# Kernel optimization log

Hardware: AMD Instinct MI355X
Metric: run time of the kernel (lower is better)

Reference implementation:

```python
import jax, jax.numpy as jnp
import numpy as np

EMBED_DIM = 512
NUM_HEADS = 8
QKV_DIM = 64
MS_HIDDEN = 16
COST_DIMS = 1
SCORES_DIMS = COST_DIMS + 1  # dot-product score + cost-mat score


def setup_inputs() -> dict:
    key = jax.random.key(0)
    ks = jax.random.split(key, 12)
    B, R, C = 8, 256, 256
    row_emb = jax.random.normal(ks[0], (B, R, EMBED_DIM), dtype=jnp.float32)
    col_emb = jax.random.normal(ks[1], (B, C, EMBED_DIM), dtype=jnp.float32)
    cost_mat = jax.random.uniform(ks[2], (B, R, C, COST_DIMS), dtype=jnp.float32)
    attn_mask = jax.random.randint(ks[3], (B, R, C), 0, 2).astype(jnp.bool_)
    # learned params (stored [in, out]; torch Linear applies x @ W.T)
    s = 1.0 / np.sqrt(EMBED_DIM)
    Wq = jax.random.uniform(ks[4], (EMBED_DIM, NUM_HEADS * QKV_DIM), minval=-s, maxval=s)
    Wk = jax.random.uniform(ks[5], (EMBED_DIM, NUM_HEADS * QKV_DIM), minval=-s, maxval=s)
    Wv = jax.random.uniform(ks[6], (EMBED_DIM, NUM_HEADS * QKV_DIM), minval=-s, maxval=s)
    Wo = jax.random.uniform(ks[7], (EMBED_DIM, EMBED_DIM), minval=-s, maxval=s)
    m1 = np.sqrt(1.0 / SCORES_DIMS)
    m2 = np.sqrt(1.0 / MS_HIDDEN)
    W1 = jax.random.uniform(ks[8], (SCORES_DIMS * NUM_HEADS, MS_HIDDEN * NUM_HEADS), minval=-m1, maxval=m1)
    W2 = jax.random.uniform(ks[9], (MS_HIDDEN * NUM_HEADS, NUM_HEADS), minval=-m2, maxval=m2)
    alpha = jnp.ones((1, NUM_HEADS, 1, 1, 1), dtype=jnp.float32)
    return {"row_emb": row_emb, "col_emb": col_emb, "cost_mat": cost_mat,
            "attn_mask": attn_mask, "Wq": Wq, "Wk": Wk, "Wv": Wv, "Wo": Wo,
            "W1": W1, "W2": W2, "alpha": alpha}


def reference(row_emb, col_emb, cost_mat, attn_mask, Wq, Wk, Wv, Wo, W1, W2, alpha):
    B, R, E = row_emb.shape
    C = col_emb.shape[1]
    H, D = NUM_HEADS, QKV_DIM
    norm = 1.0 / jnp.sqrt(jnp.asarray(D, row_emb.dtype))
    # projections -> (b, h, s, d)
    q = (row_emb @ Wq).reshape(B, R, H, D).transpose(0, 2, 1, 3)
    k = (col_emb @ Wk).reshape(B, C, H, D).transpose(0, 2, 1, 3)
    v = (col_emb @ Wv).reshape(B, C, H, D).transpose(0, 2, 1, 3)
    dot = norm * jnp.einsum('bhrd,bhcd->bhrc', q, k)  # (B,H,R,C)
    # mixed-score MLP: concat dot score with alpha-scaled cost-mat score
    cm = alpha * cost_mat[:, None]                    # (B,H,R,C,COST_DIMS)
    scores = jnp.concatenate([dot[..., None], cm], axis=-1)  # (B,H,R,C,S)
    s = scores.transpose(0, 2, 3, 1, 4).reshape(B, R, C, H * SCORES_DIMS)
    mixed = jax.nn.relu(s @ W1) @ W2                  # (B,R,C,H)
    logits = mixed.transpose(0, 3, 1, 2)              # (B,H,R,C)
    # masked softmax (rows fully masked -> zero weights)
    mask = attn_mask[:, None]                         # (B,1,R,C)
    all_masked = jnp.all(mask, axis=-1, keepdims=True)
    logits = jnp.where(mask, -jnp.inf, logits)
    weights = jax.nn.softmax(logits, axis=-1)
    weights = jnp.where(all_masked, 0.0, weights)
    out = jnp.einsum('bhrc,bhcd->bhrd', weights, v)   # (B,H,R,D)
    out = out.transpose(0, 2, 1, 3).reshape(B, R, H * D)
    return out @ Wo
```

## Files before the change

### kernel.cpp

```cpp
#include <hip/hip_runtime.h>
#include <hip/hip_bf16.h>

#define B_ 8
#define R_ 256
#define C_ 256
#define H_ 8
#define D_ 64

typedef __attribute__((ext_vector_type(8))) short s8v;
typedef __attribute__((ext_vector_type(4))) short s4v;
typedef __attribute__((ext_vector_type(4))) float f4v;

static __device__ __forceinline__ unsigned short f2b(float x) {
    __hip_bfloat16 h = __float2bfloat16(x);
    return *reinterpret_cast<unsigned short*>(&h);
}
static __device__ __forceinline__ float b2f(unsigned short u) {
    union { unsigned int i; float f; } c;
    c.i = (unsigned int)u << 16;
    return c.f;
}

__global__ __launch_bounds__(256) void prep(
    const float* __restrict__ re, const float* __restrict__ ce,
    const float* __restrict__ W1, const float* __restrict__ W2,
    const float* __restrict__ alpha,
    unsigned short* __restrict__ reb, unsigned short* __restrict__ ceb,
    unsigned short* __restrict__ w1af, unsigned short* __restrict__ w2af)
{
    const int t = blockIdx.x * 256 + threadIdx.x;
    {
        float2 v = *(const float2*)&re[(size_t)t * 2];
        reb[t * 2]     = f2b(v.x);
        reb[t * 2 + 1] = f2b(v.y);
        float2 w = *(const float2*)&ce[(size_t)t * 2];
        ceb[t * 2]     = f2b(w.x);
        ceb[t * 2 + 1] = f2b(w.y);
    }
    if (blockIdx.x == 0) {
        const int l = threadIdx.x;
        for (int q = 0; q < 16; ++q) {
            const int idx = l * 16 + q;
            const int kk = idx & 7, lane = (idx >> 3) & 63, n = idx >> 9;
            const int j = n * 16 + (lane & 15);
            const int s = 8 * (lane >> 4) + kk;
            float val = 0.f;
            if (s < 16) {
                val = W1[(2 * (s >> 1)) * 128 + j];
            } else if (s < 18) {
                for (int h = 0; h < 8; ++h)
                    val += alpha[h] * W1[(2 * h + 1) * 128 + j];
            }
            w1af[idx] = f2b(val);
        }
        for (int q = 0; q < 8; ++q) {
            const int idx = l * 8 + q;
            const int kk = idx & 7, lane = (idx >> 3) & 63, kc = idx >> 9;
            const int h = lane & 15, g = lane >> 4;
            const int phi = 16 * (2 * kc + (kk >> 2)) + 4 * g + (kk & 3);
            w2af[idx] = f2b(h < 8 ? W2[phi * 8 + h] : 0.f);
        }
    }
}

__global__ __launch_bounds__(256) void prep_w(
    const float* __restrict__ Wq, const float* __restrict__ Wk,
    const float* __restrict__ Wv, const float* __restrict__ Wo,
    unsigned short* __restrict__ wqt, unsigned short* __restrict__ wkt,
    unsigned short* __restrict__ wvt, unsigned short* __restrict__ wot)
{
    __shared__ unsigned short ldsT[64][68];
    const int which = blockIdx.y;
    const float* W = which == 0 ? Wq : which == 1 ? Wk : which == 2 ? Wv : Wo;
    unsigned short* WT = which == 0 ? wqt : which == 1 ? wkt : which == 2 ? wvt : wot;
    const int k0 = (blockIdx.x & 7) * 64;
    const int n0 = (blockIdx.x >> 3) * 64;
    const int t = threadIdx.x;
    const int rn = t & 15;
    const int rk = t >> 4;
    #pragma unroll
    for (int i = 0; i < 4; ++i) {
        const int kk = rk + 16 * i;
        const float4 v = *(const float4*)&W[(size_t)(k0 + kk) * 512 + n0 + rn * 4];
        ldsT[rn * 4 + 0][kk] = f2b(v.x);
        ldsT[rn * 4 + 1][kk] = f2b(v.y);
        ldsT[rn * 4 + 2][kk] = f2b(v.z);
        ldsT[rn * 4 + 3][kk] = f2b(v.w);
    }
    __syncthreads();
    #pragma unroll
    for (int i = 0; i < 4; ++i) {
        const int nn = rk + 16 * i;
        const s4v r = *(const s4v*)&ldsT[nn][rn * 4];
        *(s4v*)&WT[(size_t)(n0 + nn) * 512 + k0 + rn * 4] = r;
    }
}

__global__ __launch_bounds__(256) void gemm_qkv(
    const unsigned short* __restrict__ reb, const unsigned short* __restrict__ ceb,
    const unsigned short* __restrict__ wqt, const unsigned short* __restrict__ wkt,
    const unsigned short* __restrict__ wvt,
    unsigned short* __restrict__ Qb, unsigned short* __restrict__ Kb,
    unsigned short* __restrict__ VT)
{
    const int z = blockIdx.z;
    const unsigned short* A;
    const unsigned short* Bm;
    int Ar0, Br0;
    if (z == 0)      { A = reb; Bm = wqt; Ar0 = blockIdx.x * 64; Br0 = blockIdx.y * 64; }
    else if (z == 1) { A = ceb; Bm = wkt; Ar0 = blockIdx.x * 64; Br0 = blockIdx.y * 64; }
    else             { A = wvt; Bm = ceb; Ar0 = blockIdx.y * 64; Br0 = blockIdx.x * 64; }

    const int t = threadIdx.x, lane = t & 63, wave = t >> 6;
    const int row0 = Ar0 + (wave >> 1) * 32;
    const int col0 = Br0 + (wave & 1) * 32;
    const int lr = lane & 15, ko = (lane >> 4) * 8;

    const unsigned short* Ap0 = A + (size_t)(row0 + lr) * 512 + ko;
    const unsigned short* Ap1 = Ap0 + 16 * 512;
    const unsigned short* Bp0 = Bm + (size_t)(col0 + lr) * 512 + ko;
    const unsigned short* Bp1 = Bp0 + 16 * 512;

    f4v acc[2][2] = {};
    #pragma unroll 4
    for (int k0 = 0; k0 < 512; k0 += 32) {
        s8v a0 = *(const s8v*)(Ap0 + k0);
        s8v a1 = *(const s8v*)(Ap1 + k0);
        s8v b0 = *(const s8v*)(Bp0 + k0);
        s8v b1 = *(const s8v*)(Bp1 + k0);
        acc[0][0] = __builtin_amdgcn_mfma_f32_16x16x32_bf16(a0, b0, acc[0][0], 0, 0, 0);
        acc[0][1] = __builtin_amdgcn_mfma_f32_16x16x32_bf16(a0, b1, acc[0][1], 0, 0, 0);
        acc[1][0] = __builtin_amdgcn_mfma_f32_16x16x32_bf16(a1, b0, acc[1][0], 0, 0, 0);
        acc[1][1] = __builtin_amdgcn_mfma_f32_16x16x32_bf16(a1, b1, acc[1][1], 0, 0, 0);
    }

    const float sc = (z == 0) ? 0.125f : 1.0f;
    const int rbase = (lane >> 4) * 4;
    #pragma unroll
    for (int i = 0; i < 2; ++i)
        #pragma unroll
        for (int j = 0; j < 2; ++j)
            #pragma unroll
            for (int reg = 0; reg < 4; ++reg) {
                const int rowIdx = row0 + i * 16 + rbase + reg;
                const int colIdx = col0 + j * 16 + lr;
                const unsigned short v = f2b(acc[i][j][reg] * sc);
                if (z == 0) {
                    Qb[(size_t)rowIdx * 512 + colIdx] = v;
                } else if (z == 1) {
                    const int b = rowIdx >> 8, c = rowIdx & 255;
                    const int h = colIdx >> 6, d = colIdx & 63;
                    Kb[(((size_t)b * 8 + h) * 256 + c) * 64 + d] = v;
                } else {
                    const int h = rowIdx >> 6, d = rowIdx & 63;
                    const int b = colIdx >> 8, c = colIdx & 255;
                    VT[(((size_t)b * 8 + h) * 64 + d) * 256 + c] = v;
                }
            }
}

__global__ __launch_bounds__(256) void gemm_out(
    const unsigned short* __restrict__ OHb, const unsigned short* __restrict__ wot,
    float* __restrict__ out)
{
    const int t = threadIdx.x, lane = t & 63, wave = t >> 6;
    const int row0 = blockIdx.x * 64 + (wave >> 1) * 32;
    const int col0 = blockIdx.y * 64 + (wave & 1) * 32;
    const int lr = lane & 15, ko = (lane >> 4) * 8;

    const unsigned short* Ap0 = OHb + (size_t)(row0 + lr) * 512 + ko;
    const unsigned short* Ap1 = Ap0 + 16 * 512;
    const unsigned short* Bp0 = wot + (size_t)(col0 + lr) * 512 + ko;
    const unsigned short* Bp1 = Bp0 + 16 * 512;

    f4v acc[2][2] = {};
    #pragma unroll 4
    for (int k0 = 0; k0 < 512; k0 += 32) {
        s8v a0 = *(const s8v*)(Ap0 + k0);
        s8v a1 = *(const s8v*)(Ap1 + k0);
        s8v b0 = *(const s8v*)(Bp0 + k0);
        s8v b1 = *(const s8v*)(Bp1 + k0);
        acc[0][0] = __builtin_amdgcn_mfma_f32_16x16x32_bf16(a0, b0, acc[0][0], 0, 0, 0);
        acc[0][1] = __builtin_amdgcn_mfma_f32_16x16x32_bf16(a0, b1, acc[0][1], 0, 0, 0);
        acc[1][0] = __builtin_amdgcn_mfma_f32_16x16x32_bf16(a1, b0, acc[1][0], 0, 0, 0);
        acc[1][1] = __builtin_amdgcn_mfma_f32_16x16x32_bf16(a1, b1, acc[1][1], 0, 0, 0);
    }

    const int rbase = (lane >> 4) * 4;
    #pragma unroll
    for (int i = 0; i < 2; ++i)
        #pragma unroll
        for (int j = 0; j < 2; ++j)
            #pragma unroll
            for (int reg = 0; reg < 4; ++reg)
                out[(size_t)(row0 + i * 16 + rbase + reg) * 512 + col0 + j * 16 + lr] =
                    acc[i][j][reg];
}

__global__ __launch_bounds__(512, 2) void attn_fused(
    const unsigned short* __restrict__ Qb,
    const unsigned short* __restrict__ Kb,
    const unsigned short* __restrict__ VT,
    const float* __restrict__ cost,
    const int* __restrict__ mask,
    const unsigned short* __restrict__ w1af,
    const unsigned short* __restrict__ w2af,
    unsigned short* __restrict__ OHb)
{
    __shared__ unsigned short dotb[4][256][24];
    __shared__ unsigned short w_t3[8][4][264];

    const int t    = threadIdx.x;
    const int lane = t & 63;
    const int w    = t >> 6;
    const int li   = lane & 15;
    const int g    = lane >> 4;
    const int b    = blockIdx.y;
    const int r0   = blockIdx.x * 4;

    {
        const int rr = lane & 3;
        const int ko = g * 8;
        const unsigned short* Qp = Qb + ((size_t)b * R_ + r0 + rr) * 512 + w * 64 + ko;
        const s8v a0 = *(const s8v*)Qp;
        const s8v a1 = *(const s8v*)(Qp + 32);
        const unsigned short* Kp = Kb + (((size_t)b * 8 + w) * 256) * 64;
        #pragma unroll
        for (int ct = 0; ct < 16; ++ct) {
            const unsigned short* Bp = Kp + (size_t)(ct * 16 + li) * 64 + ko;
            const s8v b0 = *(const s8v*)Bp;
            const s8v b1v = *(const s8v*)(Bp + 32);
            f4v acc = __builtin_amdgcn_mfma_f32_16x16x32_bf16(a0, b0, (f4v){0.f,0.f,0.f,0.f}, 0, 0, 0);
            acc = __builtin_amdgcn_mfma_f32_16x16x32_bf16(a1, b1v, acc, 0, 0, 0);
            if (lane < 16) {
                const int c = ct * 16 + lane;
                #pragma unroll
                for (int reg = 0; reg < 4; ++reg) {
                    const float x = acc[reg];
                    const unsigned short hi = f2b(x);
                    const unsigned short lo = f2b(x - b2f(hi));
                    *(unsigned int*)&dotb[reg][c][2 * w] =
                        (unsigned int)hi | ((unsigned int)lo << 16);
                }
            }
        }
    }
    __syncthreads();

    {
        s8v w1A[8], w2A[4];
        #pragma unroll
        for (int n = 0; n < 8; ++n) w1A[n] = ((const s8v*)w1af)[n * 64 + lane];
        #pragma unroll
        for (int kc = 0; kc < 4; ++kc) w2A[kc] = ((const s8v*)w2af)[kc * 64 + lane];

        const int r   = w & 3;
        const int ct0 = (w >> 2) * 8;
        const float* costRow = cost + ((size_t)b * R_ + r0 + r) * 256;

        #pragma unroll
        for (int i = 0; i < 8; ++i) {
            const int c = (ct0 + i) * 16 + li;
            s8v b1;
            {
                const s8v t0 = *(const s8v*)&dotb[r][c][(g & 1) * 8];
                const float cv = costRow[c];
                const unsigned short chi = f2b(cv);
                const unsigned short clo = f2b(cv - b2f(chi));
                if (g < 2) {
                    b1 = t0;
                } else if (g == 2) {
                    s8v bc = {0, 0, 0, 0, 0, 0, 0, 0};
                    bc[0] = (short)chi; bc[1] = (short)clo;
                    b1 = bc;
                } else {
                    s8v bz = {0, 0, 0, 0, 0, 0, 0, 0};
                    b1 = bz;
                }
            }
            unsigned int pk[16];
            #pragma unroll
            for (int n = 0; n < 8; ++n) {
                f4v acc = __builtin_amdgcn_mfma_f32_16x16x32_bf16(
                    w1A[n], b1, (f4v){0.f,0.f,0.f,0.f}, 0, 0, 0);
                const float a0 = fmaxf(acc[0], 0.f), a1 = fmaxf(acc[1], 0.f);
                const float a2 = fmaxf(acc[2], 0.f), a3 = fmaxf(acc[3], 0.f);
                pk[2 * n]     = (unsigned int)f2b(a0) | ((unsigned int)f2b(a1) << 16);
                pk[2 * n + 1] = (unsigned int)f2b(a2) | ((unsigned int)f2b(a3) << 16);
            }
            f4v acc2 = (f4v){0.f, 0.f, 0.f, 0.f};
            #pragma unroll
            for (int kc = 0; kc < 4; ++kc) {
                union { s8v v; unsigned int u[4]; } bb;
                bb.u[0] = pk[4 * kc + 0];
                bb.u[1] = pk[4 * kc + 1];
                bb.u[2] = pk[4 * kc + 2];
                bb.u[3] = pk[4 * kc + 3];
                acc2 = __builtin_amdgcn_mfma_f32_16x16x32_bf16(w2A[kc], bb.v, acc2, 0, 0, 0);
            }
            if (g < 2) {
                float* lp = (float*)&dotb[r][c][0];
                #pragma unroll
                for (int reg = 0; reg < 4; ++reg)
                    lp[4 * g + reg] = acc2[reg];
            }
        }
    }
    __syncthreads();

    {
        #pragma unroll
        for (int p = 0; p < 4; ++p) {
            const int idx = w * 4 + p;
            const int r = idx >> 3, h = idx & 7;
            const int4 mk = *(const int4*)&mask[((size_t)b * R_ + r0 + r) * 256 + lane * 4];
            float v[4];
            #pragma unroll
            for (int i = 0; i < 4; ++i)
                v[i] = ((const float*)&dotb[r][lane * 4 + i][0])[h];
            const bool m0 = mk.x != 0, m1 = mk.y != 0;
            const bool m2 = mk.z != 0, m3 = mk.w != 0;
            const float v0 = m0 ? -INFINITY : v[0];
            const float v1 = m1 ? -INFINITY : v[1];
            const float v2 = m2 ? -INFINITY : v[2];
            const float v3 = m3 ? -INFINITY : v[3];
            float mx = fmaxf(fmaxf(v0, v1), fmaxf(v2, v3));
            #pragma unroll
            for (int off = 32; off >= 1; off >>= 1)
                mx = fmaxf(mx, __shfl_xor(mx, off));
            const float e0 = m0 ? 0.f : __expf(v0 - mx);
            const float e1 = m1 ? 0.f : __expf(v1 - mx);
            const float e2 = m2 ? 0.f : __expf(v2 - mx);
            const float e3 = m3 ? 0.f : __expf(v3 - mx);
            float sm = e0 + e1 + e2 + e3;
            #pragma unroll
            for (int off = 32; off >= 1; off >>= 1)
                sm += __shfl_xor(sm, off);
            const float inv = sm > 0.f ? 1.0f / sm : 0.f;
            s4v pk;
            pk[0] = (short)f2b(e0 * inv);
            pk[1] = (short)f2b(e1 * inv);
            pk[2] = (short)f2b(e2 * inv);
            pk[3] = (short)f2b(e3 * inv);
            *(s4v*)&w_t3[h][r][lane * 4] = pk;
        }
    }
    __syncthreads();

    {
        s8v bfr[8];
        #pragma unroll
        for (int kt = 0; kt < 8; ++kt)
            bfr[kt] = *(const s8v*)&w_t3[w][li & 3][kt * 32 + g * 8];
        const unsigned short* Vp = VT + (((size_t)b * 8 + w) * 64) * 256;
        #pragma unroll
        for (int dt = 0; dt < 4; ++dt) {
            const unsigned short* Ap = Vp + (size_t)(dt * 16 + li) * 256 + g * 8;
            f4v acc = (f4v){0.f, 0.f, 0.f, 0.f};
            #pragma unroll
            for (int kt = 0; kt < 8; ++kt)
                acc = __builtin_amdgcn_mfma_f32_16x16x32_bf16(
                    *(const s8v*)(Ap + kt * 32), bfr[kt], acc, 0, 0, 0);
            if (li < 4) {
                s4v o;
                o[0] = (short)f2b(acc[0]);
                o[1] = (short)f2b(acc[1]);
                o[2] = (short)f2b(acc[2]);
                o[3] = (short)f2b(acc[3]);
                *(s4v*)&OHb[((size_t)b * R_ + r0 + li) * 512 + w * 64 + dt * 16 + 4 * g] = o;
            }
        }
    }
}

extern "C" void kernel_launch(void* const* d_in, const int* in_sizes, int n_in,
                              void* d_out, int out_size, void* d_ws, size_t ws_size,
                              hipStream_t stream)
{
    const float* row_emb = (const float*)d_in[0];
    const float* col_emb = (const float*)d_in[1];
    const float* cost    = (const float*)d_in[2];
    const int*   mask    = (const int*)d_in[3];
    const float* Wq = (const float*)d_in[4];
    const float* Wk = (const float*)d_in[5];
    const float* Wv = (const float*)d_in[6];
    const float* Wo = (const float*)d_in[7];
    const float* W1 = (const float*)d_in[8];
    const float* W2 = (const float*)d_in[9];
    const float* alpha = (const float*)d_in[10];
    float* out = (float*)d_out;

    unsigned short* base = (unsigned short*)d_ws;
    unsigned short* Qb   = base;
    unsigned short* Kb   = base + 1048576;
    unsigned short* VT   = base + 2097152;
    unsigned short* OHb  = base + 3145728;
    unsigned short* reb  = base + 4194304;
    unsigned short* ceb  = base + 5242880;
    unsigned short* wqt  = base + 6291456;
    unsigned short* wkt  = base + 6553600;
    unsigned short* wvt  = base + 6815744;
    unsigned short* wot  = base + 7077888;
    unsigned short* w1af = base + 7340032;
    unsigned short* w2af = base + 7344128;

    prep<<<2048, 256, 0, stream>>>(row_emb, col_emb, W1, W2, alpha,
                                   reb, ceb, w1af, w2af);
    prep_w<<<dim3(64, 4), 256, 0, stream>>>(Wq, Wk, Wv, Wo, wqt, wkt, wvt, wot);
    gemm_qkv<<<dim3(32, 8, 3), 256, 0, stream>>>(reb, ceb, wqt, wkt, wvt,
                                                 Qb, Kb, VT);
    attn_fused<<<dim3(64, 8), 512, 0, stream>>>(Qb, Kb, VT, cost, mask,
                                                w1af, w2af, OHb);
    gemm_out<<<dim3(32, 8), 256, 0, stream>>>(OHb, wot, out);
}
```

Before: 93.37 us.

## Merge weight prep into prep kernel, shrink out-GEMM tiles, stage MLP weights in LDS

Folds the weight transpose/convert kernel into the main prep kernel as extra blocks, which removes one kernel launch. Halves the rows per block in the output GEMM so it launches twice as many blocks for better CU occupancy. In the attention kernel, the mixed-score MLP weights move from per-wave registers into shared memory, and the cost and mask loads are issued early to overlap with the Q/K work. The trade-off is more LDS use and extra LDS reads inside the MLP loop, in return for lower register pressure and earlier memory latency.

```diff
diff --git a/kernel.cpp b/kernel.cpp
--- a/kernel.cpp
+++ b/kernel.cpp
@@ -25,9 +25,43 @@
     const float* __restrict__ re, const float* __restrict__ ce,
     const float* __restrict__ W1, const float* __restrict__ W2,
     const float* __restrict__ alpha,
+    const float* __restrict__ Wq, const float* __restrict__ Wk,
+    const float* __restrict__ Wv, const float* __restrict__ Wo,
     unsigned short* __restrict__ reb, unsigned short* __restrict__ ceb,
-    unsigned short* __restrict__ w1af, unsigned short* __restrict__ w2af)
+    unsigned short* __restrict__ w1af, unsigned short* __restrict__ w2af,
+    unsigned short* __restrict__ wqt, unsigned short* __restrict__ wkt,
+    unsigned short* __restrict__ wvt, unsigned short* __restrict__ wot)
 {
+    __shared__ unsigned short ldsT[64][68];
+    if (blockIdx.x >= 2048) {
+        const int bb = blockIdx.x - 2048;
+        const int which = bb >> 6;
+        const float* W = which == 0 ? Wq : which == 1 ? Wk : which == 2 ? Wv : Wo;
+        unsigned short* WT = which == 0 ? wqt : which == 1 ? wkt : which == 2 ? wvt : wot;
+        const int k0 = (bb & 7) * 64;
+        const int n0 = ((bb >> 3) & 7) * 64;
+        const int tt = threadIdx.x;
+        const int rn = tt & 15;
+        const int rk = tt >> 4;
+        #pragma unroll
+        for (int i = 0; i < 4; ++i) {
+            const int kk = rk + 16 * i;
+            const float4 v = *(const float4*)&W[(size_t)(k0 + kk) * 512 + n0 + rn * 4];
+            ldsT[rn * 4 + 0][kk] = f2b(v.x);
+            ldsT[rn * 4 + 1][kk] = f2b(v.y);
+            ldsT[rn * 4 + 2][kk] = f2b(v.z);
+            ldsT[rn * 4 + 3][kk] = f2b(v.w);
+        }
+        __syncthreads();
+        #pragma unroll
+        for (int i = 0; i < 4; ++i) {
+            const int nn = rk + 16 * i;
+            const s4v r = *(const s4v*)&ldsT[nn][rn * 4];
+            *(s4v*)&WT[(size_t)(n0 + nn) * 512 + k0 + rn * 4] = r;
+        }
+        return;
+    }
+
     const int t = blockIdx.x * 256 + threadIdx.x;
     {
         float2 v = *(const float2*)&re[(size_t)t * 2];
@@ -60,39 +94,6 @@
             const int phi = 16 * (2 * kc + (kk >> 2)) + 4 * g + (kk & 3);
             w2af[idx] = f2b(h < 8 ? W2[phi * 8 + h] : 0.f);
         }
-    }
-}
-
-__global__ __launch_bounds__(256) void prep_w(
-    const float* __restrict__ Wq, const float* __restrict__ Wk,
-    const float* __restrict__ Wv, const float* __restrict__ Wo,
-    unsigned short* __restrict__ wqt, unsigned short* __restrict__ wkt,
-    unsigned short* __restrict__ wvt, unsigned short* __restrict__ wot)
-{
-    __shared__ unsigned short ldsT[64][68];
-    const int which = blockIdx.y;
-    const float* W = which == 0 ? Wq : which == 1 ? Wk : which == 2 ? Wv : Wo;
-    unsigned short* WT = which == 0 ? wqt : which == 1 ? wkt : which == 2 ? wvt : wot;
-    const int k0 = (blockIdx.x & 7) * 64;
-    const int n0 = (blockIdx.x >> 3) * 64;
-    const int t = threadIdx.x;
-    const int rn = t & 15;
-    const int rk = t >> 4;
-    #pragma unroll
-    for (int i = 0; i < 4; ++i) {
-        const int kk = rk + 16 * i;
-        const float4 v = *(const float4*)&W[(size_t)(k0 + kk) * 512 + n0 + rn * 4];
-        ldsT[rn * 4 + 0][kk] = f2b(v.x);
-        ldsT[rn * 4 + 1][kk] = f2b(v.y);
-        ldsT[rn * 4 + 2][kk] = f2b(v.z);
-        ldsT[rn * 4 + 3][kk] = f2b(v.w);
-    }
-    __syncthreads();
-    #pragma unroll
-    for (int i = 0; i < 4; ++i) {
-        const int nn = rk + 16 * i;
-        const s4v r = *(const s4v*)&ldsT[nn][rn * 4];
-        *(s4v*)&WT[(size_t)(n0 + nn) * 512 + k0 + rn * 4] = r;
     }
 }
 
@@ -164,37 +165,30 @@
     float* __restrict__ out)
 {
     const int t = threadIdx.x, lane = t & 63, wave = t >> 6;
-    const int row0 = blockIdx.x * 64 + (wave >> 1) * 32;
-    const int col0 = blockIdx.y * 64 + (wave & 1) * 32;
+    const int row0 = blockIdx.x * 32 + (wave & 1) * 16;
+    const int col0 = blockIdx.y * 64 + (wave >> 1) * 32;
     const int lr = lane & 15, ko = (lane >> 4) * 8;
 
     const unsigned short* Ap0 = OHb + (size_t)(row0 + lr) * 512 + ko;
-    const unsigned short* Ap1 = Ap0 + 16 * 512;
     const unsigned short* Bp0 = wot + (size_t)(col0 + lr) * 512 + ko;
     const unsigned short* Bp1 = Bp0 + 16 * 512;
 
-    f4v acc[2][2] = {};
+    f4v acc[2] = {};
     #pragma unroll 4
     for (int k0 = 0; k0 < 512; k0 += 32) {
         s8v a0 = *(const s8v*)(Ap0 + k0);
-        s8v a1 = *(const s8v*)(Ap1 + k0);
         s8v b0 = *(const s8v*)(Bp0 + k0);
         s8v b1 = *(const s8v*)(Bp1 + k0);
-        acc[0][0] = __builtin_amdgcn_mfma_f32_16x16x32_bf16(a0, b0, acc[0][0], 0, 0, 0);
-        acc[0][1] = __builtin_amdgcn_mfma_f32_16x16x32_bf16(a0, b1, acc[0][1], 0, 0, 0);
-        acc[1][0] = __builtin_amdgcn_mfma_f32_16x16x32_bf16(a1, b0, acc[1][0], 0, 0, 0);
-        acc[1][1] = __builtin_amdgcn_mfma_f32_16x16x32_bf16(a1, b1, acc[1][1], 0, 0, 0);
+        acc[0] = __builtin_amdgcn_mfma_f32_16x16x32_bf16(a0, b0, acc[0], 0, 0, 0);
+        acc[1] = __builtin_amdgcn_mfma_f32_16x16x32_bf16(a0, b1, acc[1], 0, 0, 0);
     }
 
     const int rbase = (lane >> 4) * 4;
     #pragma unroll
-    for (int i = 0; i < 2; ++i)
-        #pragma unroll
-        for (int j = 0; j < 2; ++j)
-            #pragma unroll
-            for (int reg = 0; reg < 4; ++reg)
-                out[(size_t)(row0 + i * 16 + rbase + reg) * 512 + col0 + j * 16 + lr] =
-                    acc[i][j][reg];
+    for (int j = 0; j < 2; ++j)
+        #pragma unroll
+        for (int reg = 0; reg < 4; ++reg)
+            out[(size_t)(row0 + rbase + reg) * 512 + col0 + j * 16 + lr] = acc[j][reg];
 }
 
 __global__ __launch_bounds__(512, 2) void attn_fused(
@@ -209,6 +203,8 @@
 {
     __shared__ unsigned short dotb[4][256][24];
     __shared__ unsigned short w_t3[8][4][264];
+    __shared__ unsigned short ws1[4096];
+    __shared__ unsigned short ws2[2048];
 
     const int t    = threadIdx.x;
     const int lane = t & 63;
@@ -217,6 +213,25 @@
     const int g    = lane >> 4;
     const int b    = blockIdx.y;
     const int r0   = blockIdx.x * 4;
+
+    ((s8v*)ws1)[t] = ((const s8v*)w1af)[t];
+    if (t < 256) ((s8v*)ws2)[t] = ((const s8v*)w2af)[t];
+
+    const int rB  = w & 3;
+    const int ct0 = (w >> 2) * 8;
+    float costv[8];
+    {
+        const float* costRow = cost + ((size_t)b * R_ + r0 + rB) * 256;
+        #pragma unroll
+        for (int i = 0; i < 8; ++i)
+            costv[i] = costRow[(ct0 + i) * 16 + li];
+    }
+    int4 mk4[4];
+    #pragma unroll
+    for (int p = 0; p < 4; ++p) {
+        const int idx = w * 4 + p;
+        mk4[p] = *(const int4*)&mask[((size_t)b * R_ + r0 + (idx >> 3)) * 256 + lane * 4];
+    }
 
     {
         const int rr = lane & 3;
@@ -248,23 +263,13 @@
     __syncthreads();
 
     {
-        s8v w1A[8], w2A[4];
-        #pragma unroll
-        for (int n = 0; n < 8; ++n) w1A[n] = ((const s8v*)w1af)[n * 64 + lane];
-        #pragma unroll
-        for (int kc = 0; kc < 4; ++kc) w2A[kc] = ((const s8v*)w2af)[kc * 64 + lane];
-
-        const int r   = w & 3;
-        const int ct0 = (w >> 2) * 8;
-        const float* costRow = cost + ((size_t)b * R_ + r0 + r) * 256;
-
         #pragma unroll
         for (int i = 0; i < 8; ++i) {
             const int c = (ct0 + i) * 16 + li;
             s8v b1;
             {
-                const s8v t0 = *(const s8v*)&dotb[r][c][(g & 1) * 8];
-                const float cv = costRow[c];
+                const s8v t0 = *(const s8v*)&dotb[rB][c][(g & 1) * 8];
+                const float cv = costv[i];
                 const unsigned short chi = f2b(cv);
                 const unsigned short clo = f2b(cv - b2f(chi));
                 if (g < 2) {
@@ -281,8 +286,9 @@
             unsigned int pk[16];
             #pragma unroll
             for (int n = 0; n < 8; ++n) {
+                const s8v w1A = *(const s8v*)&ws1[(n * 64 + lane) * 8];
                 f4v acc = __builtin_amdgcn_mfma_f32_16x16x32_bf16(
-                    w1A[n], b1, (f4v){0.f,0.f,0.f,0.f}, 0, 0, 0);
+                    w1A, b1, (f4v){0.f,0.f,0.f,0.f}, 0, 0, 0);
                 const float a0 = fmaxf(acc[0], 0.f), a1 = fmaxf(acc[1], 0.f);
                 const float a2 = fmaxf(acc[2], 0.f), a3 = fmaxf(acc[3], 0.f);
                 pk[2 * n]     = (unsigned int)f2b(a0) | ((unsigned int)f2b(a1) << 16);
@@ -291,15 +297,16 @@
             f4v acc2 = (f4v){0.f, 0.f, 0.f, 0.f};
             #pragma unroll
             for (int kc = 0; kc < 4; ++kc) {
+                const s8v w2A = *(const s8v*)&ws2[(kc * 64 + lane) * 8];
                 union { s8v v; unsigned int u[4]; } bb;
                 bb.u[0] = pk[4 * kc + 0];
                 bb.u[1] = pk[4 * kc + 1];
                 bb.u[2] = pk[4 * kc + 2];
                 bb.u[3] = pk[4 * kc + 3];
-                acc2 = __builtin_amdgcn_mfma_f32_16x16x32_bf16(w2A[kc], bb.v, acc2, 0, 0, 0);
+                acc2 = __builtin_amdgcn_mfma_f32_16x16x32_bf16(w2A, bb.v, acc2, 0, 0, 0);
             }
             if (g < 2) {
-                float* lp = (float*)&dotb[r][c][0];
+                float* lp = (float*)&dotb[rB][c][0];
                 #pragma unroll
                 for (int reg = 0; reg < 4; ++reg)
                     lp[4 * g + reg] = acc2[reg];
@@ -313,7 +320,7 @@
         for (int p = 0; p < 4; ++p) {
             const int idx = w * 4 + p;
             const int r = idx >> 3, h = idx & 7;
-            const int4 mk = *(const int4*)&mask[((size_t)b * R_ + r0 + r) * 256 + lane * 4];
+            const int4 mk = mk4[p];
             float v[4];
             #pragma unroll
             for (int i = 0; i < 4; ++i)
@@ -404,12 +411,12 @@
     unsigned short* w1af = base + 7340032;
     unsigned short* w2af = base + 7344128;
 
-    prep<<<2048, 256, 0, stream>>>(row_emb, col_emb, W1, W2, alpha,
-                                   reb, ceb, w1af, w2af);
-    prep_w<<<dim3(64, 4), 256, 0, stream>>>(Wq, Wk, Wv, Wo, wqt, wkt, wvt, wot);
+    prep<<<2304, 256, 0, stream>>>(row_emb, col_emb, W1, W2, alpha,
+                                   Wq, Wk, Wv, Wo,
+                                   reb, ceb, w1af, w2af, wqt, wkt, wvt, wot);
     gemm_qkv<<<dim3(32, 8, 3), 256, 0, stream>>>(reb, ceb, wqt, wkt, wvt,
                                                  Qb, Kb, VT);
     attn_fused<<<dim3(64, 8), 512, 0, stream>>>(Qb, Kb, VT, cost, mask,
                                                 w1af, w2af, OHb);
-    gemm_out<<<dim3(32, 8), 256, 0, stream>>>(OHb, wot, out);
-}
+    gemm_out<<<dim3(64, 8), 256, 0, stream>>>(OHb, wot, out);
+}
```

Result: no change. 91.60 us (-1.9%).
